# Optimization experiments

Measured on AMD Instinct MI355X. Metric: run time of the kernel, lower is better.

The kernel has to match this reference:

```python
import jax, jax.numpy as jnp
import numpy as np

VOCAB, EMB = 100000, 128
KERNEL_NUM, SIGMA, EXACT_SIGMA = 21, 0.1, 0.001
OUT_LAYERS = [10, 5]

def _mus_sigmas():
    step = 2.0 / (KERNEL_NUM - 1)
    mus = [1.0, 1.0 - step / 2]
    for i in range(1, KERNEL_NUM - 1):
        mus.append(mus[i] - step)
    mus = list(reversed(mus))  # [-0.95, ..., 0.95, 1.0]
    sigmas = [SIGMA] * (KERNEL_NUM - 1) + [EXACT_SIGMA]
    return mus, sigmas

MUS, SIGMAS = _mus_sigmas()

def setup_inputs() -> dict:
    key = jax.random.key(0)
    ks = jax.random.split(key, 12)
    B, Q, D = 1024, 64, 256
    q1 = jax.random.randint(ks[0], (B, Q), 0, VOCAB, dtype=jnp.int32)
    d1 = jax.random.randint(ks[1], (B, D), 0, VOCAB, dtype=jnp.int32)
    q2 = jax.random.randint(ks[2], (B, Q), 0, VOCAB, dtype=jnp.int32)
    d2 = jax.random.randint(ks[3], (B, D), 0, VOCAB, dtype=jnp.int32)
    emb = jax.random.normal(ks[4], (VOCAB, EMB), dtype=jnp.float32)
    emb = emb.at[0].set(0.0)  # padding_idx=0
    dims = [KERNEL_NUM] + OUT_LAYERS + [1]
    W1 = jax.random.normal(ks[5], (dims[0], dims[1]), dtype=jnp.float32) / np.sqrt(dims[0])
    b1 = jnp.zeros((dims[1],), dtype=jnp.float32)
    W2 = jax.random.normal(ks[6], (dims[1], dims[2]), dtype=jnp.float32) / np.sqrt(dims[1])
    b2 = jnp.zeros((dims[2],), dtype=jnp.float32)
    W3 = jax.random.normal(ks[7], (dims[2], dims[3]), dtype=jnp.float32) / np.sqrt(dims[2])
    b3 = jnp.zeros((dims[3],), dtype=jnp.float32)
    return {"q1": q1, "d1": d1, "q2": q2, "d2": d2, "emb": emb,
            "W1": W1, "b1": b1, "W2": W2, "b2": b2, "W3": W3, "b3": b3}

def _matching_matrix(emb, q_ids, d_ids):
    q = emb[q_ids]  # [B,Q,E]
    d = emb[d_ids]  # [B,D,E]
    qn = q / (jnp.linalg.norm(q, axis=-1, keepdims=True) + 1e-13)
    dn = d / (jnp.linalg.norm(d, axis=-1, keepdims=True) + 1e-13)
    return jnp.einsum('bqe,bde->bqd', qn, dn)  # [B,Q,D]

def _apply_kernels(M):
    KM = []
    for mu, sig in zip(MUS, SIGMAS):
        k = jnp.exp(-(M - mu) ** 2 / (2.0 * sig ** 2))
        KM.append(jnp.log1p(k.sum(axis=-1)).sum(axis=-1))  # [B]
    return jnp.stack(KM, axis=-1)  # [B,21]

def _mlp(x, W1, b1, W2, b2, W3, b3):
    # _get_mlp puts ReLU BEFORE each Linear
    x = jax.nn.relu(x) @ W1 + b1
    x = jax.nn.relu(x) @ W2 + b2
    x = jax.nn.relu(x) @ W3 + b3
    return x  # [B,1]

def _predict(emb, q, d, W1, b1, W2, b2, W3, b3):
    M = _matching_matrix(emb, q, d)
    ko = _apply_kernels(M)
    return _mlp(ko, W1, b1, W2, b2, W3, b3)

def reference(q1, d1, q2, d2, emb, W1, b1, W2, b2, W3, b3):
    l1 = _predict(emb, q1, d1, W1, b1, W2, b2, W3, b3)
    l2 = _predict(emb, q2, d2, W1, b1, W2, b2, W3, b3)
    return jax.nn.sigmoid(l1 - l2)  # [B,1]
```

## Files before the change

kernel.cpp:

```cpp
#include <hip/hip_runtime.h>


typedef __attribute__((ext_vector_type(8))) short bf16x8;
typedef __attribute__((ext_vector_type(4))) float f32x4;
typedef __attribute__((ext_vector_type(2))) float f32x2;

__device__ __forceinline__ unsigned short f2bf(float f) {
    unsigned u = __float_as_uint(f);
    u += 0x7fffu + ((u >> 16) & 1u);
    return (unsigned short)(u >> 16);
}
__device__ __forceinline__ float bf2f(unsigned short h) {
    return __uint_as_float(((unsigned)h) << 16);
}

__global__ __launch_bounds__(256)
void norm_split_kernel(const float* __restrict__ emb,
                       unsigned short* __restrict__ th,
                       unsigned short* __restrict__ tl, int vocab)
{
    const int row = blockIdx.x * 8 + (threadIdx.x >> 5);
    if (row >= vocab) return;
    const int ln = threadIdx.x & 31;
    const float4 v = *reinterpret_cast<const float4*>(emb + (size_t)row * 128 + ln * 4);
    float ss = v.x*v.x + v.y*v.y + v.z*v.z + v.w*v.w;
    #pragma unroll
    for (int m = 16; m >= 1; m >>= 1) ss += __shfl_xor(ss, m);
    const float rn = 1.0f / (sqrtf(ss) + 1e-13f);
    const float f0 = v.x*rn, f1 = v.y*rn, f2 = v.z*rn, f3 = v.w*rn;
    const unsigned short h0 = f2bf(f0), h1 = f2bf(f1), h2 = f2bf(f2), h3 = f2bf(f3);
    const unsigned short g0 = f2bf(f0 - bf2f(h0)), g1 = f2bf(f1 - bf2f(h1));
    const unsigned short g2 = f2bf(f2 - bf2f(h2)), g3 = f2bf(f3 - bf2f(h3));
    const int off = row * 128 + ln * 4;
    *reinterpret_cast<uint2*>(th + off) =
        make_uint2((unsigned)h0 | ((unsigned)h1 << 16), (unsigned)h2 | ((unsigned)h3 << 16));
    *reinterpret_cast<uint2*>(tl + off) =
        make_uint2((unsigned)g0 | ((unsigned)g1 << 16), (unsigned)g2 | ((unsigned)g3 << 16));
}

__device__ __forceinline__ void glds16(const unsigned short* g, unsigned short* l) {
    __builtin_amdgcn_global_load_lds((const __attribute__((address_space(1))) void*)g,
                                     (__attribute__((address_space(3))) void*)l, 16, 0, 0);
}

__device__ __forceinline__ void stage_pre_d(const unsigned short* __restrict__ th,
                                            const unsigned short* __restrict__ tl,
                                            const int* __restrict__ ids, int base,
                                            unsigned short* __restrict__ dh,
                                            unsigned short* __restrict__ dl,
                                            int w, int l)
{
    #pragma unroll
    for (int j = 0; j < 2; j++) {
        const int r   = 8*w + 4*j + (l >> 4);
        const int id  = ids[base + r];
        const int gsw = ((l & 15) ^ (r & 15)) << 3;
        glds16(th + (size_t)id * 128 + gsw, dh + (8*w + 4*j) * 128);
        glds16(tl + (size_t)id * 128 + gsw, dl + (8*w + 4*j) * 128);
    }
}

__device__ __forceinline__ void stage_pre_q(const unsigned short* __restrict__ th,
                                            const unsigned short* __restrict__ tl,
                                            const int* __restrict__ qids,
                                            unsigned short* __restrict__ h0b, unsigned short* __restrict__ l0b,
                                            unsigned short* __restrict__ h1b, unsigned short* __restrict__ l1b,
                                            int w, int l)
{
    unsigned short* dh = (w >> 1) ? h1b : h0b;
    unsigned short* dl = (w >> 1) ? l1b : l0b;
    const int rb = (w & 1) * 16;
    #pragma unroll
    for (int j = 0; j < 4; j++) {
        const int r   = rb + 4*j + (l >> 4);
        const int id  = qids[(w >> 1) * 32 + r];
        const int gsw = ((l & 15) ^ (r & 15)) << 3;
        glds16(th + (size_t)id * 128 + gsw, dh + (rb + 4*j) * 128);
        glds16(tl + (size_t)id * 128 + gsw, dl + (rb + 4*j) * 128);
    }
}

#define PKF(a, b, c) __builtin_elementwise_fma((a), (b), (c))

__device__ __forceinline__ void apply_pair(float m0, float m1, f32x2 (&sp)[21]) {
    const f32x2 m2 = {m0, m1};
    const f32x2 dm = m2 - 0.05f;
    const f32x2 ta = (dm * dm) * -72.13475204444817f;
    const f32x2 x2 = m2 * 14.426950408889634f;
    const f32x2 t0 = { __builtin_amdgcn_exp2f(ta[0]), __builtin_amdgcn_exp2f(ta[1]) };
    const f32x2 R  = { __builtin_amdgcn_exp2f(x2[0]), __builtin_amdgcn_exp2f(x2[1]) };
    const f32x2 Ri = { __builtin_amdgcn_exp2f(-x2[0]), __builtin_amdgcn_exp2f(-x2[1]) };
    sp[10] += t0;
    f32x2 tu = t0;
    tu *= R;  sp[11] = PKF(tu, (f32x2)3.6787944117e-1f,  sp[11]);
    tu *= R;  sp[12] = PKF(tu, (f32x2)4.9787068368e-2f,  sp[12]);
    tu *= R;  sp[13] = PKF(tu, (f32x2)2.4787521767e-3f,  sp[13]);
    tu *= R;  sp[14] = PKF(tu, (f32x2)4.5399929762e-5f,  sp[14]);
    tu *= R;  sp[15] = PKF(tu, (f32x2)3.0590232050e-7f,  sp[15]);
    tu *= R;  sp[16] = PKF(tu, (f32x2)7.5825604279e-10f, sp[16]);
    tu *= R;  sp[17] = PKF(tu, (f32x2)6.9144001069e-13f, sp[17]);
    tu *= R;  sp[18] = PKF(tu, (f32x2)2.3195228302e-16f, sp[18]);
    tu *= R;  sp[19] = PKF(tu, (f32x2)2.8625185805e-20f, sp[19]);
    f32x2 td = t0;
    td *= Ri; sp[9] += td;
    td *= Ri; sp[8] = PKF(td, (f32x2)3.6787944117e-1f,  sp[8]);
    td *= Ri; sp[7] = PKF(td, (f32x2)4.9787068368e-2f,  sp[7]);
    td *= Ri; sp[6] = PKF(td, (f32x2)2.4787521767e-3f,  sp[6]);
    td *= Ri; sp[5] = PKF(td, (f32x2)4.5399929762e-5f,  sp[5]);
    td *= Ri; sp[4] = PKF(td, (f32x2)3.0590232050e-7f,  sp[4]);
    td *= Ri; sp[3] = PKF(td, (f32x2)7.5825604279e-10f, sp[3]);
    td *= Ri; sp[2] = PKF(td, (f32x2)6.9144001069e-13f, sp[2]);
    td *= Ri; sp[1] = PKF(td, (f32x2)2.3195228302e-16f, sp[1]);
    td *= Ri; sp[0] = PKF(td, (f32x2)2.8625185805e-20f, sp[0]);
    const f32x2 e  = m2 - 1.0f;
    const f32x2 ea = (e * e) * -721347.5204444817f;
    const f32x2 ex = { __builtin_amdgcn_exp2f(ea[0]), __builtin_amdgcn_exp2f(ea[1]) };
    sp[20] += ex;
}

#define MFMA(a, b, c) __builtin_amdgcn_mfma_f32_16x16x32_bf16((a), (b), (c), 0, 0, 0)

__global__ __launch_bounds__(256, 2)
void knrm_main(const int* __restrict__ q1, const int* __restrict__ d1,
               const int* __restrict__ q2, const int* __restrict__ d2,
               const unsigned short* __restrict__ th, const unsigned short* __restrict__ tl,
               float* __restrict__ kmws)
{
    __shared__ unsigned short bh[3][32*128];
    __shared__ unsigned short bl[3][32*128];
    __shared__ int   sh_ids[256];
    __shared__ float KMpart[4][21];

    const int tid = threadIdx.x;
    const int bb  = blockIdx.x >> 1;
    const int p   = blockIdx.x & 1;
    const int w   = tid >> 6;
    const int l   = tid & 63;
    const int lr  = l & 15;
    const int lh  = l >> 4;

    const int* qids = (p == 0 ? q1 : q2) + bb * 64;
    const int* dids = (p == 0 ? d1 : d2) + bb * 256;

    sh_ids[tid] = dids[tid];
    stage_pre_q(th, tl, qids, bh[0], bl[0], bh[1], bl[1], w, l);
    asm volatile("s_waitcnt vmcnt(0) lgkmcnt(0)" ::: "memory");
    __builtin_amdgcn_s_barrier();

    bf16x8 Bh[4], Bl[4];
    {
        const unsigned short* qh = (w >> 1) ? bh[1] : bh[0];
        const unsigned short* ql = (w >> 1) ? bl[1] : bl[0];
        const int qr = (w * 16 + lr) & 31;
        #pragma unroll
        for (int ks = 0; ks < 4; ks++) {
            const int off = qr*128 + (((ks*4 + lh) ^ lr) << 3);
            Bh[ks] = *reinterpret_cast<const bf16x8*>(qh + off);
            Bl[ks] = *reinterpret_cast<const bf16x8*>(ql + off);
        }
    }
    asm volatile("s_waitcnt lgkmcnt(0)" ::: "memory");
    __builtin_amdgcn_s_barrier();

    f32x2 sp[21];
    #pragma unroll
    for (int i = 0; i < 21; i++) sp[i] = (f32x2){0.f, 0.f};

    stage_pre_d(th, tl, sh_ids, 0,  bh[0], bl[0], w, l);
    stage_pre_d(th, tl, sh_ids, 32, bh[1], bl[1], w, l);
    stage_pre_d(th, tl, sh_ids, 64, bh[2], bl[2], w, l);

    for (int c = 0; c < 8; c++) {
        if (c < 6)      asm volatile("s_waitcnt vmcnt(8)" ::: "memory");
        else if (c == 6) asm volatile("s_waitcnt vmcnt(4)" ::: "memory");
        else             asm volatile("s_waitcnt vmcnt(0)" ::: "memory");
        __builtin_amdgcn_s_barrier();

        const unsigned short* ch = bh[c % 3];
        const unsigned short* cl = bl[c % 3];
        f32x4 C0 = {0.f,0.f,0.f,0.f}, C1 = {0.f,0.f,0.f,0.f};
        #pragma unroll
        for (int ks = 0; ks < 4; ks++) {
            const int o0 = lr*128        + (((ks*4 + lh) ^ lr) << 3);
            const int o1 = (16 + lr)*128 + (((ks*4 + lh) ^ lr) << 3);
            const bf16x8 A0h = *reinterpret_cast<const bf16x8*>(ch + o0);
            const bf16x8 A0l = *reinterpret_cast<const bf16x8*>(cl + o0);
            const bf16x8 A1h = *reinterpret_cast<const bf16x8*>(ch + o1);
            const bf16x8 A1l = *reinterpret_cast<const bf16x8*>(cl + o1);
            C0 = MFMA(A0h, Bh[ks], C0); C1 = MFMA(A1h, Bh[ks], C1);
            C0 = MFMA(A0h, Bl[ks], C0); C1 = MFMA(A1h, Bl[ks], C1);
            C0 = MFMA(A0l, Bh[ks], C0); C1 = MFMA(A1l, Bh[ks], C1);
        }
        #pragma unroll
        for (int r = 0; r < 4; r++) apply_pair(C0[r], C1[r], sp);

        __builtin_amdgcn_s_barrier();
        if (c < 5)
            stage_pre_d(th, tl, sh_ids, (c + 3) * 32, bh[(c + 3) % 3], bl[(c + 3) % 3], w, l);
    }

    #pragma unroll
    for (int i = 0; i < 21; i++) {
        float s = sp[i][0] + sp[i][1];
        s += __shfl_xor(s, 16);
        s += __shfl_xor(s, 32);
        float t = log1pf(s);
        t += __shfl_xor(t, 1);
        t += __shfl_xor(t, 2);
        t += __shfl_xor(t, 4);
        t += __shfl_xor(t, 8);
        if (l == 0) KMpart[w][i] = t;
    }
    __syncthreads();
    if (tid < 21)
        kmws[blockIdx.x * 21 + tid] = KMpart[0][tid] + KMpart[1][tid]
                                    + KMpart[2][tid] + KMpart[3][tid];
}

__global__ __launch_bounds__(64)
void mlp_kernel(const float* __restrict__ kmws,
                const float* __restrict__ W1, const float* __restrict__ b1,
                const float* __restrict__ W2, const float* __restrict__ b2,
                const float* __restrict__ W3, const float* __restrict__ b3,
                float* __restrict__ out)
{
    __shared__ float KMs[2][21], x1s[2][10], x2s[2][5];
    const int tid = threadIdx.x;
    const int bb  = blockIdx.x;
    if (tid < 42) KMs[tid / 21][tid % 21] = kmws[(bb * 2 + tid / 21) * 21 + (tid % 21)];
    __syncthreads();
    if (tid < 10) {
        for (int p = 0; p < 2; p++) {
            float acc = b1[tid];
            #pragma unroll
            for (int i = 0; i < 21; i++) acc = fmaf(fmaxf(KMs[p][i], 0.0f), W1[i*10 + tid], acc);
            x1s[p][tid] = acc;
        }
    }
    __syncthreads();
    if (tid < 5) {
        for (int p = 0; p < 2; p++) {
            float acc = b2[tid];
            #pragma unroll
            for (int i = 0; i < 10; i++) acc = fmaf(fmaxf(x1s[p][i], 0.0f), W2[i*5 + tid], acc);
            x2s[p][tid] = acc;
        }
    }
    __syncthreads();
    if (tid == 0) {
        float lv[2];
        for (int p = 0; p < 2; p++) {
            float acc = b3[0];
            #pragma unroll
            for (int i = 0; i < 5; i++) acc = fmaf(fmaxf(x2s[p][i], 0.0f), W3[i], acc);
            lv[p] = acc;
        }
        out[bb] = 1.0f / (1.0f + expf(lv[1] - lv[0]));
    }
}

__device__ __forceinline__ void stage_f32(const float* __restrict__ emb,
                                          const int* __restrict__ ids,
                                          unsigned short* __restrict__ hi,
                                          unsigned short* __restrict__ lo,
                                          int tid)
{
    const int lg = tid >> 5;
    const int ln = tid & 31;
    #pragma unroll
    for (int i = 0; i < 4; i++) {
        const int row = i * 8 + lg;
        const int id  = ids[row];
        const float4 v = *reinterpret_cast<const float4*>(emb + (size_t)id * 128 + ln * 4);
        float ss = v.x*v.x + v.y*v.y + v.z*v.z + v.w*v.w;
        #pragma unroll
        for (int m = 16; m >= 1; m >>= 1) ss += __shfl_xor(ss, m);
        const float rn = 1.0f / (sqrtf(ss) + 1e-13f);
        const float f0 = v.x*rn, f1 = v.y*rn, f2 = v.z*rn, f3 = v.w*rn;
        const unsigned short h0 = f2bf(f0), h1 = f2bf(f1), h2 = f2bf(f2), h3 = f2bf(f3);
        const unsigned short g0 = f2bf(f0 - bf2f(h0)), g1 = f2bf(f1 - bf2f(h1));
        const unsigned short g2 = f2bf(f2 - bf2f(h2)), g3 = f2bf(f3 - bf2f(h3));
        const int off = row*128 + (((ln >> 1) ^ (row & 15)) << 3) + ((ln & 1) << 2);
        *reinterpret_cast<uint2*>(hi + off) =
            make_uint2((unsigned)h0 | ((unsigned)h1 << 16), (unsigned)h2 | ((unsigned)h3 << 16));
        *reinterpret_cast<uint2*>(lo + off) =
            make_uint2((unsigned)g0 | ((unsigned)g1 << 16), (unsigned)g2 | ((unsigned)g3 << 16));
    }
}

__global__ __launch_bounds__(256, 2)
void knrm_fallback(const int* __restrict__ q1, const int* __restrict__ d1,
                   const int* __restrict__ q2, const int* __restrict__ d2,
                   const float* __restrict__ emb,
                   const float* __restrict__ W1, const float* __restrict__ b1,
                   const float* __restrict__ W2, const float* __restrict__ b2,
                   const float* __restrict__ W3, const float* __restrict__ b3,
                   float* __restrict__ out)
{
    __shared__ unsigned short bh[2][32*128], bl[2][32*128];
    __shared__ float KMpart[2][4][21];
    __shared__ float x1s[2][10], x2s[2][5];
    const int tid = threadIdx.x;
    const int bb  = blockIdx.x;
    const int w   = tid >> 6;
    const int l   = tid & 63;
    const int lr  = l & 15;
    const int lh  = l >> 4;

    for (int p = 0; p < 2; p++) {
        const int* qids = (p == 0 ? q1 : q2) + bb * 64;
        const int* dids = (p == 0 ? d1 : d2) + bb * 256;
        stage_f32(emb, qids,      bh[0], bl[0], tid);
        stage_f32(emb, qids + 32, bh[1], bl[1], tid);
        __syncthreads();
        bf16x8 Bh[4], Bl[4];
        const int qb = w >> 1;
        const int qr = (w * 16 + lr) & 31;
        #pragma unroll
        for (int ks = 0; ks < 4; ks++) {
            const int off = qr*128 + (((ks*4 + lh) ^ lr) << 3);
            Bh[ks] = *reinterpret_cast<const bf16x8*>(&bh[qb][off]);
            Bl[ks] = *reinterpret_cast<const bf16x8*>(&bl[qb][off]);
        }
        __syncthreads();
        f32x2 sp[21];
        #pragma unroll
        for (int i = 0; i < 21; i++) sp[i] = (f32x2){0.f, 0.f};
        for (int c = 0; c < 8; c++) {
            stage_f32(emb, dids + c * 32, bh[c & 1], bl[c & 1], tid);
            __syncthreads();
            const unsigned short* ch = bh[c & 1];
            const unsigned short* cl = bl[c & 1];
            f32x4 C0 = {0.f,0.f,0.f,0.f}, C1 = {0.f,0.f,0.f,0.f};
            #pragma unroll
            for (int ks = 0; ks < 4; ks++) {
                const int o0 = lr*128        + (((ks*4 + lh) ^ lr) << 3);
                const int o1 = (16 + lr)*128 + (((ks*4 + lh) ^ lr) << 3);
                const bf16x8 A0h = *reinterpret_cast<const bf16x8*>(ch + o0);
                const bf16x8 A0l = *reinterpret_cast<const bf16x8*>(cl + o0);
                const bf16x8 A1h = *reinterpret_cast<const bf16x8*>(ch + o1);
                const bf16x8 A1l = *reinterpret_cast<const bf16x8*>(cl + o1);
                C0 = MFMA(A0h, Bh[ks], C0); C1 = MFMA(A1h, Bh[ks], C1);
                C0 = MFMA(A0h, Bl[ks], C0); C1 = MFMA(A1h, Bl[ks], C1);
                C0 = MFMA(A0l, Bh[ks], C0); C1 = MFMA(A1l, Bh[ks], C1);
            }
            #pragma unroll
            for (int r = 0; r < 4; r++) apply_pair(C0[r], C1[r], sp);
            __syncthreads();
        }
        #pragma unroll
        for (int i = 0; i < 21; i++) {
            float s = sp[i][0] + sp[i][1];
            s += __shfl_xor(s, 16);
            s += __shfl_xor(s, 32);
            float t = log1pf(s);
            t += __shfl_xor(t, 1);
            t += __shfl_xor(t, 2);
            t += __shfl_xor(t, 4);
            t += __shfl_xor(t, 8);
            if (l == 0) KMpart[p][w][i] = t;
        }
    }
    __syncthreads();
    if (tid < 10) {
        for (int p = 0; p < 2; p++) {
            float acc = b1[tid];
            #pragma unroll
            for (int i = 0; i < 21; i++) {
                const float km = KMpart[p][0][i] + KMpart[p][1][i]
                               + KMpart[p][2][i] + KMpart[p][3][i];
                acc = fmaf(fmaxf(km, 0.0f), W1[i*10 + tid], acc);
            }
            x1s[p][tid] = acc;
        }
    }
    __syncthreads();
    if (tid < 5) {
        for (int p = 0; p < 2; p++) {
            float acc = b2[tid];
            #pragma unroll
            for (int i = 0; i < 10; i++) acc = fmaf(fmaxf(x1s[p][i], 0.0f), W2[i*5 + tid], acc);
            x2s[p][tid] = acc;
        }
    }
    __syncthreads();
    if (tid == 0) {
        float lv[2];
        for (int p = 0; p < 2; p++) {
            float acc = b3[0];
            #pragma unroll
            for (int i = 0; i < 5; i++) acc = fmaf(fmaxf(x2s[p][i], 0.0f), W3[i], acc);
            lv[p] = acc;
        }
        out[bb] = 1.0f / (1.0f + expf(lv[1] - lv[0]));
    }
}

extern "C" void kernel_launch(void* const* d_in, const int* in_sizes, int n_in,
                              void* d_out, int out_size, void* d_ws, size_t ws_size,
                              hipStream_t stream)
{
    const int*   q1  = (const int*)  d_in[0];
    const int*   d1  = (const int*)  d_in[1];
    const int*   q2  = (const int*)  d_in[2];
    const int*   d2  = (const int*)  d_in[3];
    const float* emb = (const float*)d_in[4];
    const float* W1  = (const float*)d_in[5];
    const float* b1  = (const float*)d_in[6];
    const float* W2  = (const float*)d_in[7];
    const float* b2  = (const float*)d_in[8];
    const float* W3  = (const float*)d_in[9];
    const float* b3  = (const float*)d_in[10];
    float* out = (float*)d_out;
    (void)n_in;

    const int    vocab = in_sizes[4] / 128;
    const size_t tabsz = (size_t)vocab * 128 * 2;
    const size_t kmsz  = (size_t)out_size * 2 * 21 * 4;
    const size_t need  = tabsz * 2 + kmsz;

    if (ws_size >= need) {
        unsigned short* th = (unsigned short*)d_ws;
        unsigned short* tl = th + (size_t)vocab * 128;
        float* kmws = (float*)((char*)d_ws + tabsz * 2);
        norm_split_kernel<<<(vocab + 7) / 8, 256, 0, stream>>>(emb, th, tl, vocab);
        knrm_main<<<out_size * 2, 256, 0, stream>>>(q1, d1, q2, d2, th, tl, kmws);
        mlp_kernel<<<out_size, 64, 0, stream>>>(kmws, W1, b1, W2, b2, W3, b3, out);
    } else {
        knrm_fallback<<<out_size, 256, 0, stream>>>(q1, d1, q2, d2, emb,
                                                    W1, b1, W2, b2, W3, b3, out);
    }
}
```

Baseline: 122.9 us.

## Shrink document chunks to 16 rows with four-slot LDS ring buffer

Each pipeline step now handles a 16-row document chunk instead of 32, over 16 iterations. A four-slot LDS ring replaces the three-slot one, keeping three chunks of prefetch in flight. Each wave stages and holds only its own 16 query rows, and issues one MFMA accumulator chain per chunk instead of two. This cuts LDS use and per-wave registers, which may allow more overlap, but doubles the number of barriers and halves the independent MFMA work between them.

```diff
diff --git a/kernel.cpp b/kernel.cpp
--- a/kernel.cpp
+++ b/kernel.cpp
@@ -43,40 +43,34 @@
                                      (__attribute__((address_space(3))) void*)l, 16, 0, 0);
 }
 
-__device__ __forceinline__ void stage_pre_d(const unsigned short* __restrict__ th,
-                                            const unsigned short* __restrict__ tl,
-                                            const int* __restrict__ ids, int base,
-                                            unsigned short* __restrict__ dh,
-                                            unsigned short* __restrict__ dl,
-                                            int w, int l)
-{
-    #pragma unroll
-    for (int j = 0; j < 2; j++) {
-        const int r   = 8*w + 4*j + (l >> 4);
-        const int id  = ids[base + r];
-        const int gsw = ((l & 15) ^ (r & 15)) << 3;
-        glds16(th + (size_t)id * 128 + gsw, dh + (8*w + 4*j) * 128);
-        glds16(tl + (size_t)id * 128 + gsw, dl + (8*w + 4*j) * 128);
-    }
-}
-
-__device__ __forceinline__ void stage_pre_q(const unsigned short* __restrict__ th,
-                                            const unsigned short* __restrict__ tl,
-                                            const int* __restrict__ qids,
-                                            unsigned short* __restrict__ h0b, unsigned short* __restrict__ l0b,
-                                            unsigned short* __restrict__ h1b, unsigned short* __restrict__ l1b,
-                                            int w, int l)
-{
-    unsigned short* dh = (w >> 1) ? h1b : h0b;
-    unsigned short* dl = (w >> 1) ? l1b : l0b;
-    const int rb = (w & 1) * 16;
+__device__ __forceinline__ void stage_d16(const unsigned short* __restrict__ th,
+                                          const unsigned short* __restrict__ tl,
+                                          const int* __restrict__ ids, int base,
+                                          unsigned short* __restrict__ dh,
+                                          unsigned short* __restrict__ dl,
+                                          int w, int l)
+{
+    const int r   = 4*w + (l >> 4);
+    const int id  = ids[base + r];
+    const int gsw = ((l & 15) ^ r) << 3;
+    glds16(th + (size_t)id * 128 + gsw, dh + 4*w * 128);
+    glds16(tl + (size_t)id * 128 + gsw, dl + 4*w * 128);
+}
+
+__device__ __forceinline__ void stage_q16(const unsigned short* __restrict__ th,
+                                          const unsigned short* __restrict__ tl,
+                                          const int* __restrict__ qids,
+                                          unsigned short* __restrict__ dh,
+                                          unsigned short* __restrict__ dl,
+                                          int w, int l)
+{
     #pragma unroll
     for (int j = 0; j < 4; j++) {
-        const int r   = rb + 4*j + (l >> 4);
-        const int id  = qids[(w >> 1) * 32 + r];
-        const int gsw = ((l & 15) ^ (r & 15)) << 3;
-        glds16(th + (size_t)id * 128 + gsw, dh + (rb + 4*j) * 128);
-        glds16(tl + (size_t)id * 128 + gsw, dl + (rb + 4*j) * 128);
+        const int r   = 4*j + (l >> 4);
+        const int id  = qids[16*w + r];
+        const int gsw = ((l & 15) ^ r) << 3;
+        glds16(th + (size_t)id * 128 + gsw, dh + 4*j * 128);
+        glds16(tl + (size_t)id * 128 + gsw, dl + 4*j * 128);
     }
 }
 
@@ -126,8 +120,8 @@
                const unsigned short* __restrict__ th, const unsigned short* __restrict__ tl,
                float* __restrict__ kmws)
 {
-    __shared__ unsigned short bh[3][32*128];
-    __shared__ unsigned short bl[3][32*128];
+    __shared__ unsigned short bh[4][16*128];
+    __shared__ unsigned short bl[4][16*128];
     __shared__ int   sh_ids[256];
     __shared__ float KMpart[4][21];
 
@@ -143,60 +137,52 @@
     const int* dids = (p == 0 ? d1 : d2) + bb * 256;
 
     sh_ids[tid] = dids[tid];
-    stage_pre_q(th, tl, qids, bh[0], bl[0], bh[1], bl[1], w, l);
+    stage_q16(th, tl, qids, bh[w], bl[w], w, l);
     asm volatile("s_waitcnt vmcnt(0) lgkmcnt(0)" ::: "memory");
     __builtin_amdgcn_s_barrier();
 
     bf16x8 Bh[4], Bl[4];
-    {
-        const unsigned short* qh = (w >> 1) ? bh[1] : bh[0];
-        const unsigned short* ql = (w >> 1) ? bl[1] : bl[0];
-        const int qr = (w * 16 + lr) & 31;
+    #pragma unroll
+    for (int ks = 0; ks < 4; ks++) {
+        const int off = lr*128 + (((ks*4 + lh) ^ lr) << 3);
+        Bh[ks] = *reinterpret_cast<const bf16x8*>(&bh[w][off]);
+        Bl[ks] = *reinterpret_cast<const bf16x8*>(&bl[w][off]);
+    }
+    asm volatile("s_waitcnt lgkmcnt(0)" ::: "memory");
+    __builtin_amdgcn_s_barrier();
+
+    f32x2 sp[21];
+    #pragma unroll
+    for (int i = 0; i < 21; i++) sp[i] = (f32x2){0.f, 0.f};
+
+    stage_d16(th, tl, sh_ids, 0,  bh[0], bl[0], w, l);
+    stage_d16(th, tl, sh_ids, 16, bh[1], bl[1], w, l);
+    stage_d16(th, tl, sh_ids, 32, bh[2], bl[2], w, l);
+
+    for (int c = 0; c < 16; c++) {
+        if (c <= 13)      asm volatile("s_waitcnt vmcnt(4)" ::: "memory");
+        else if (c == 14) asm volatile("s_waitcnt vmcnt(2)" ::: "memory");
+        else              asm volatile("s_waitcnt vmcnt(0)" ::: "memory");
+        __builtin_amdgcn_s_barrier();
+
+        const unsigned short* ch = bh[c & 3];
+        const unsigned short* cl = bl[c & 3];
+        f32x4 C = {0.f,0.f,0.f,0.f};
         #pragma unroll
         for (int ks = 0; ks < 4; ks++) {
-            const int off = qr*128 + (((ks*4 + lh) ^ lr) << 3);
-            Bh[ks] = *reinterpret_cast<const bf16x8*>(qh + off);
-            Bl[ks] = *reinterpret_cast<const bf16x8*>(ql + off);
-        }
-    }
-    asm volatile("s_waitcnt lgkmcnt(0)" ::: "memory");
-    __builtin_amdgcn_s_barrier();
-
-    f32x2 sp[21];
-    #pragma unroll
-    for (int i = 0; i < 21; i++) sp[i] = (f32x2){0.f, 0.f};
-
-    stage_pre_d(th, tl, sh_ids, 0,  bh[0], bl[0], w, l);
-    stage_pre_d(th, tl, sh_ids, 32, bh[1], bl[1], w, l);
-    stage_pre_d(th, tl, sh_ids, 64, bh[2], bl[2], w, l);
-
-    for (int c = 0; c < 8; c++) {
-        if (c < 6)      asm volatile("s_waitcnt vmcnt(8)" ::: "memory");
-        else if (c == 6) asm volatile("s_waitcnt vmcnt(4)" ::: "memory");
-        else             asm volatile("s_waitcnt vmcnt(0)" ::: "memory");
+            const int o = lr*128 + (((ks*4 + lh) ^ lr) << 3);
+            const bf16x8 Ah = *reinterpret_cast<const bf16x8*>(ch + o);
+            const bf16x8 Al = *reinterpret_cast<const bf16x8*>(cl + o);
+            C = MFMA(Ah, Bh[ks], C);
+            C = MFMA(Ah, Bl[ks], C);
+            C = MFMA(Al, Bh[ks], C);
+        }
+        apply_pair(C[0], C[1], sp);
+        apply_pair(C[2], C[3], sp);
+
         __builtin_amdgcn_s_barrier();
-
-        const unsigned short* ch = bh[c % 3];
-        const unsigned short* cl = bl[c % 3];
-        f32x4 C0 = {0.f,0.f,0.f,0.f}, C1 = {0.f,0.f,0.f,0.f};
-        #pragma unroll
-        for (int ks = 0; ks < 4; ks++) {
-            const int o0 = lr*128        + (((ks*4 + lh) ^ lr) << 3);
-            const int o1 = (16 + lr)*128 + (((ks*4 + lh) ^ lr) << 3);
-            const bf16x8 A0h = *reinterpret_cast<const bf16x8*>(ch + o0);
-            const bf16x8 A0l = *reinterpret_cast<const bf16x8*>(cl + o0);
-            const bf16x8 A1h = *reinterpret_cast<const bf16x8*>(ch + o1);
-            const bf16x8 A1l = *reinterpret_cast<const bf16x8*>(cl + o1);
-            C0 = MFMA(A0h, Bh[ks], C0); C1 = MFMA(A1h, Bh[ks], C1);
-            C0 = MFMA(A0h, Bl[ks], C0); C1 = MFMA(A1h, Bl[ks], C1);
-            C0 = MFMA(A0l, Bh[ks], C0); C1 = MFMA(A1l, Bh[ks], C1);
-        }
-        #pragma unroll
-        for (int r = 0; r < 4; r++) apply_pair(C0[r], C1[r], sp);
-
-        __builtin_amdgcn_s_barrier();
-        if (c < 5)
-            stage_pre_d(th, tl, sh_ids, (c + 3) * 32, bh[(c + 3) % 3], bl[(c + 3) % 3], w, l);
+        if (c <= 12)
+            stage_d16(th, tl, sh_ids, (c + 3) * 16, bh[(c + 3) & 3], bl[(c + 3) & 3], w, l);
     }
 
     #pragma unroll
```

Result: faster. 120.5 us (-2.0%).
